# Optimization experiments

Measured on AMD Instinct MI355X. Metric: run time of the kernel, lower is better.

The kernel has to match this reference:

```python
import jax, jax.numpy as jnp
import numpy as np

N, E, H = 50000, 800000, 128
HQ = H // 4  # 32


def _mlp(x, w1, b1, w2, b2):
    return jax.nn.relu(x @ w1 + b1) @ w2 + b2


def setup_inputs() -> dict:
    key = jax.random.key(0)
    ks = jax.random.split(key, 16)

    def lin(k, fan_in, fan_out):
        lim = 1.0 / np.sqrt(fan_in)
        kw, kb = jax.random.split(k)
        w = jax.random.uniform(kw, (fan_in, fan_out), jnp.float32, -lim, lim)
        b = jax.random.uniform(kb, (fan_out,), jnp.float32, -lim, lim)
        return w, b

    x = jax.random.normal(ks[0], (N, H), jnp.float32)
    pos = jax.random.normal(ks[1], (N, 3), jnp.float32)
    edge_index = jax.random.randint(ks[2], (2, E), 0, N, jnp.int64)

    pw1, pb1 = lin(ks[3], 3, HQ)
    pw2, pb2 = lin(ks[4], HQ, HQ)
    mw1, mb1 = lin(ks[5], 2 * H + HQ, H)
    mw2, mb2 = lin(ks[6], H, H)
    uw1, ub1 = lin(ks[7], 2 * H, H)
    uw2, ub2 = lin(ks[8], H, H)

    return dict(x=x, pos=pos, edge_index=edge_index,
                pw1=pw1, pb1=pb1, pw2=pw2, pb2=pb2,
                mw1=mw1, mb1=mb1, mw2=mw2, mb2=mb2,
                uw1=uw1, ub1=ub1, uw2=uw2, ub2=ub2)


def reference(x, pos, edge_index,
              pw1, pb1, pw2, pb2,
              mw1, mb1, mw2, mb2,
              uw1, ub1, uw2, ub2):
    row, col = edge_index[0], edge_index[1]
    # position features from relative positions [E, 3] -> [E, H//4]
    pos_feat = _mlp(pos[row] - pos[col], pw1, pb1, pw2, pb2)
    # per-edge messages [E, 2H + H//4] -> [E, H]
    msg_in = jnp.concatenate([x[row], x[col], pos_feat], axis=-1)
    messages = _mlp(msg_in, mw1, mb1, mw2, mb2)
    # scatter-add messages into destination nodes (index_add on col)
    agg = jax.ops.segment_sum(messages, col, num_segments=x.shape[0])
    # node update [N, 2H] -> [N, H]
    return _mlp(jnp.concatenate([x, agg], axis=-1), uw1, ub1, uw2, ub2)
```

## Files before the change

kernel.cpp:

```cpp
#include <hip/hip_runtime.h>
#include <hip/hip_bf16.h>

#define NN 50000
#define NE 800000
#define HD 128
#define SCAN_CHUNK 1024
#define SCAN_BLOCKS ((NN + SCAN_CHUNK - 1) / SCAN_CHUNK)
#define NB_NODE 1024
#define EPB ((NE + NB_NODE - 1) / NB_NODE)
#define NB_SSUB 256
#define NB_SCAT (NB_SSUB * 8)
#define EPC ((NE + NB_SSUB - 1) / NB_SSUB)
#define NPG (NN / 8)

typedef __attribute__((ext_vector_type(8))) short s16x8;
typedef __attribute__((ext_vector_type(4))) float f32x4;

static __device__ __forceinline__ unsigned short f2bf(float f) {
    unsigned int u = __float_as_uint(f);
    u = (u + 0x7FFFu + ((u >> 16) & 1u)) >> 16;
    return (unsigned short)u;
}
static __device__ __forceinline__ float bf2f(unsigned short h) {
    return __uint_as_float(((unsigned int)h) << 16);
}
static __device__ __forceinline__ unsigned int f2bf2(float lo, float hi) {
    __hip_bfloat162 h = __float22bfloat162_rn(make_float2(lo, hi));
    return *reinterpret_cast<unsigned int*>(&h);
}

#define WFENCE() do { asm volatile("s_waitcnt lgkmcnt(0)" ::: "memory"); \
                      __builtin_amdgcn_sched_barrier(0); } while (0)

__global__ __launch_bounds__(256, 3) void node_kernel(
    const float* __restrict__ x, const float* __restrict__ mw1,
    const float* __restrict__ mb1, const float* __restrict__ pb2,
    const int* __restrict__ ei,
    unsigned short* __restrict__ xa, unsigned short* __restrict__ xb,
    float* __restrict__ aggH, int* __restrict__ cnt)
{
    __shared__ __align__(16) unsigned short sB[128 * 136];
    __shared__ __align__(16) unsigned short sSt[4][16 * 132];
    __shared__ int sIdx64;

    int bid = blockIdx.x;
    int tid = threadIdx.x;

    {
        f32x4 z = {0.f, 0.f, 0.f, 0.f};
        const int total4 = NN * HD / 4;
        for (int i = bid * 256 + tid; i < total4; i += NB_NODE * 256)
            ((f32x4*)aggH)[i] = z;
    }
    if (tid == 0) {
        int z = 1;
        for (int k = 0; k < 16; ++k) if (ei[2 * k + 1] != 0) z = 0;
        sIdx64 = z;
    }
    int half = bid & 1;
    for (int idx = tid; idx < 128 * 128; idx += 256) {
        int c = idx & 127, k = idx >> 7;
        sB[c * 136 + k] = f2bf(mw1[(half * 128 + k) * 128 + c]);
    }
    __syncthreads();

    {
        int he0 = bid * EPB;
        int he1 = he0 + EPB; if (he1 > NE) he1 = NE;
        if (sIdx64) {
            for (int e = he0 + tid; e < he1; e += 256)
                atomicAdd(&cnt[ei[2 * NE + 2 * e]], 1);
        } else {
            for (int e = he0 + tid; e < he1; e += 256)
                atomicAdd(&cnt[ei[NE + e]], 1);
        }
    }

    int lane = tid & 63, wv = tid >> 6;
    int r16 = lane & 15, g4 = lane >> 4;
    unsigned short* st = sSt[wv];
    unsigned short* dst = half ? xb : xa;

    float bcr[8];
    #pragma unroll
    for (int tc = 0; tc < 8; ++tc) bcr[tc] = 0.f;
    if (half) {
        #pragma unroll
        for (int tc = 0; tc < 8; ++tc) bcr[tc] = mb1[tc * 16 + r16];
        for (int i = 0; i < 32; ++i) {
            float pv = pb2[i];
            #pragma unroll
            for (int tc = 0; tc < 8; ++tc)
                bcr[tc] = fmaf(pv, mw1[(256 + i) * 128 + tc * 16 + r16], bcr[tc]);
        }
    }

    const int NT = NN / 16;
    const int nb = NB_NODE >> 1;
    const int nbid = bid >> 1;

    for (int t = nbid * 4 + wv; t < NT; t += nb * 4) {
        int r0 = t * 16;
        int row = r0 + r16;
        s16x8 a[4];
        #pragma unroll
        for (int ks = 0; ks < 4; ++ks) {
            const float* p = &x[(size_t)row * HD + ks * 32 + g4 * 8];
            float4 v0 = *(const float4*)p;
            float4 v1 = *(const float4*)(p + 4);
            union { s16x8 v; unsigned int u[4]; } av;
            av.u[0] = f2bf2(v0.x, v0.y); av.u[1] = f2bf2(v0.z, v0.w);
            av.u[2] = f2bf2(v1.x, v1.y); av.u[3] = f2bf2(v1.z, v1.w);
            a[ks] = av.v;
        }
        float hold[4];
        #pragma unroll
        for (int tc = 0; tc < 8; ++tc) {
            int col = tc * 16 + r16;
            float bv = bcr[tc];
            f32x4 acc = {bv, bv, bv, bv};
            #pragma unroll
            for (int ks = 0; ks < 4; ++ks) {
                s16x8 b = *(const s16x8*)&sB[col * 136 + ks * 32 + g4 * 8];
                acc = __builtin_amdgcn_mfma_f32_16x16x32_bf16(a[ks], b, acc, 0, 0, 0);
            }
            if ((tc & 1) == 0) {
                #pragma unroll
                for (int j = 0; j < 4; ++j) hold[j] = acc[j];
            } else {
                #pragma unroll
                for (int j = 0; j < 4; ++j)
                    *(unsigned int*)&st[(g4 * 4 + j) * 132 + r16 * 8 + (tc - 1)] =
                        f2bf2(hold[j], acc[j]);
            }
        }
        WFENCE();
        #pragma unroll
        for (int i = 0; i < 4; ++i) {
            int idx = i * 512 + lane * 8;
            int rr = idx >> 7, cc = idx & 127;
            *(s16x8*)&dst[(size_t)(r0 + rr) * HD + cc] = *(const s16x8*)&st[rr * 132 + cc];
        }
        WFENCE();
    }
}

__global__ void scan1_kernel(const int* __restrict__ cnt, int* __restrict__ cursor,
                             int* __restrict__ bsum)
{
    __shared__ int tot[256];
    int b = blockIdx.x, t = threadIdx.x;
    int i0 = b * SCAN_CHUNK + t * 4;
    int v[4];
    #pragma unroll
    for (int k = 0; k < 4; ++k) v[k] = (i0 + k < NN) ? cnt[i0 + k] : 0;
    tot[t] = v[0] + v[1] + v[2] + v[3];
    __syncthreads();
    if (t == 0) {
        int run = 0;
        for (int i = 0; i < 256; ++i) { int x = tot[i]; tot[i] = run; run += x; }
        bsum[b] = run;
    }
    __syncthreads();
    int p = tot[t];
    #pragma unroll
    for (int k = 0; k < 4; ++k) {
        if (i0 + k < NN) cursor[i0 + k] = p;
        p += v[k];
    }
}

__global__ void scan3_kernel(int* __restrict__ cursor, const int* __restrict__ bsum,
                             const int* __restrict__ cnt, int* __restrict__ sC)
{
    __shared__ int sCarry;
    int b = blockIdx.x, t = threadIdx.x;
    if (t == 0) {
        int run = 0;
        for (int i = 0; i < b; ++i) run += bsum[i];
        sCarry = run;
    }
    __syncthreads();
    int carry = sCarry;
    int i0 = b * SCAN_CHUNK + t * 4;
    #pragma unroll
    for (int k = 0; k < 4; ++k) {
        int i = i0 + k;
        if (i < NN) {
            int s = cursor[i] + carry;
            cursor[i] = s;
            int n = cnt[i];
            for (int j = 0; j < n; ++j) sC[s + j] = i;
        }
    }
}

__global__ void scatterprep_kernel(
    const int* __restrict__ ei, int* __restrict__ cursor, int* __restrict__ sR,
    const float* __restrict__ pw2, const float* __restrict__ mw1,
    const float* __restrict__ mw2, const float* __restrict__ mb2,
    const float* __restrict__ uw1,
    float* __restrict__ Wpc, float* __restrict__ W3, float* __restrict__ b3)
{
    __shared__ int sIdx64;
    int bid = blockIdx.x, tid = threadIdx.x;

    if (bid >= NB_SCAT) {
        int rb = bid - NB_SCAT;
        if (rb == 64) {
            for (int idx = tid; idx < 32 * 128; idx += 256) {
                int j = idx >> 7, k = idx & 127;
                float s = 0.f;
                #pragma unroll 8
                for (int i = 0; i < 32; ++i) s += pw2[j * 32 + i] * mw1[(256 + i) * 128 + k];
                Wpc[idx] = s;
            }
            return;
        }
        int idx = rb * 256 + tid;
        {
            int k = idx >> 7, j = idx & 127;
            float s = 0.f;
            #pragma unroll 4
            for (int c = 0; c < 128; ++c)
                s += mw2[k * 128 + c] * uw1[(128 + c) * 128 + j];
            W3[idx] = s;
        }
        if (rb == 0 && tid < 128) {
            int j = tid;
            float s = 0.f;
            #pragma unroll 4
            for (int c = 0; c < 128; ++c)
                s += mb2[c] * uw1[(128 + c) * 128 + j];
            b3[j] = s;
        }
        return;
    }

    if (tid == 0) {
        int z = 1;
        for (int k = 0; k < 16; ++k) if (ei[2 * k + 1] != 0) z = 0;
        sIdx64 = z;
    }
    __syncthreads();

    int g = bid & 7;
    int sub = bid >> 3;
    int clo = g * NPG;
    int chi = (g == 7) ? NN : clo + NPG;
    int e0 = sub * EPC;
    int e1 = e0 + EPC; if (e1 > NE) e1 = NE;

    if (sIdx64) {
        for (int e = e0 + tid; e < e1; e += 256) {
            int c = ei[2 * NE + 2 * e];
            if (c >= clo && c < chi) {
                int r = ei[2 * e];
                int p = atomicAdd(&cursor[c], 1);
                sR[p] = r;
            }
        }
    } else {
        for (int e = e0 + tid; e < e1; e += 256) {
            int c = ei[NE + e];
            if (c >= clo && c < chi) {
                int r = ei[e];
                int p = atomicAdd(&cursor[c], 1);
                sR[p] = r;
            }
        }
    }
}

__global__ __launch_bounds__(256, 3) void edge_kernel(
    const float* __restrict__ pos,
    const int* __restrict__ sR, const int* __restrict__ sC,
    const float* __restrict__ pw1, const float* __restrict__ pb1,
    const unsigned short* __restrict__ xa, const unsigned short* __restrict__ xb,
    const float* __restrict__ Wpc,
    float* __restrict__ aggH)
{
    __shared__ __align__(16) unsigned short sT[4][16 * 136];

    int tid = threadIdx.x;
    int lane = tid & 63, wv = tid >> 6;
    int r16 = lane & 15, g4 = lane >> 4;
    unsigned short* stg = sT[wv];

    s16x8 wr[8];
    #pragma unroll
    for (int tc = 0; tc < 8; ++tc) {
        s16x8 w;
        #pragma unroll
        for (int i = 0; i < 8; ++i)
            w[i] = (short)f2bf(Wpc[(g4 * 8 + i) * 128 + tc * 16 + r16]);
        wr[tc] = w;
    }
    float pw10[8], pw11[8], pw12[8], pb1r[8];
    #pragma unroll
    for (int i = 0; i < 8; ++i) {
        int k = g4 * 8 + i;
        pw10[i] = pw1[k]; pw11[i] = pw1[32 + k]; pw12[i] = pw1[64 + k];
        pb1r[i] = pb1[k];
    }

    const int NW = gridDim.x * 4;
    const int NT = NE / 16;
    int gw = blockIdx.x * 4 + wv;
    if (gw >= NT) return;

    int2 rc, rcN;
    rc.x = sR[gw * 16 + r16];
    rc.y = sC[gw * 16 + r16];
    rcN = rc;
    if (gw + NW < NT) {
        rcN.x = sR[(gw + NW) * 16 + r16];
        rcN.y = sC[(gw + NW) * 16 + r16];
    }
    float dp0 = pos[rc.x * 3 + 0] - pos[rc.y * 3 + 0];
    float dp1 = pos[rc.x * 3 + 1] - pos[rc.y * 3 + 1];
    float dp2 = pos[rc.x * 3 + 2] - pos[rc.y * 3 + 2];
    s16x8 ga[4], gb[4];
    #pragma unroll
    for (int j = 0; j < 4; ++j) {
        int gx = __shfl(rc.x, g4 * 4 + j, 64);
        int gy = __shfl(rc.y, g4 * 4 + j, 64);
        ga[j] = *(const s16x8*)&xa[(size_t)gx * HD + r16 * 8];
        gb[j] = *(const s16x8*)&xb[(size_t)gy * HD + r16 * 8];
    }

    for (int t = gw; t < NT; t += NW) {
        bool hn  = (t + NW) < NT;
        bool hn2 = (t + 2 * NW) < NT;

        union { s16x8 v; unsigned int u[4]; } apf;
        #pragma unroll
        for (int i2 = 0; i2 < 4; ++i2) {
            int i = 2 * i2;
            float v0 = fmaf(dp0, pw10[i], fmaf(dp1, pw11[i], fmaf(dp2, pw12[i], pb1r[i])));
            float v1 = fmaf(dp0, pw10[i+1], fmaf(dp1, pw11[i+1], fmaf(dp2, pw12[i+1], pb1r[i+1])));
            apf.u[i2] = f2bf2(fmaxf(v0, 0.f), fmaxf(v1, 0.f));
        }

        float hold[4];
        #pragma unroll
        for (int tc = 0; tc < 8; ++tc) {
            f32x4 acc;
            #pragma unroll
            for (int j = 0; j < 4; ++j)
                acc[j] = bf2f((unsigned short)ga[j][tc]) + bf2f((unsigned short)gb[j][tc]);
            acc = __builtin_amdgcn_mfma_f32_16x16x32_bf16(apf.v, wr[tc], acc, 0, 0, 0);
            if ((tc & 1) == 0) {
                #pragma unroll
                for (int j = 0; j < 4; ++j) hold[j] = fmaxf(acc[j], 0.f);
            } else {
                #pragma unroll
                for (int j = 0; j < 4; ++j)
                    *(unsigned int*)&stg[(g4 * 4 + j) * 136 + r16 * 8 + (tc - 1)] =
                        f2bf2(hold[j], fmaxf(acc[j], 0.f));
            }
        }
        WFENCE();

        if (hn) {
            #pragma unroll
            for (int j = 0; j < 4; ++j) {
                int gx = __shfl(rcN.x, g4 * 4 + j, 64);
                int gy = __shfl(rcN.y, g4 * 4 + j, 64);
                ga[j] = *(const s16x8*)&xa[(size_t)gx * HD + r16 * 8];
                gb[j] = *(const s16x8*)&xb[(size_t)gy * HD + r16 * 8];
            }
        }

        int2 rcN2 = rcN;
        if (hn2) {
            int i2x = (t + 2 * NW) * 16 + r16;
            rcN2.x = sR[i2x];
            rcN2.y = sC[i2x];
        }
        float dp0N = 0.f, dp1N = 0.f, dp2N = 0.f;
        if (hn) {
            dp0N = pos[rcN.x * 3 + 0] - pos[rcN.y * 3 + 0];
            dp1N = pos[rcN.x * 3 + 1] - pos[rcN.y * 3 + 1];
            dp2N = pos[rcN.x * 3 + 2] - pos[rcN.y * 3 + 2];
        }

        {
            int tb = __builtin_amdgcn_readfirstlane(t);
            const int* __restrict__ scp = sC + tb * 16;
            int p0 = (lane & 15) * 8 + (lane >> 4);
            int p1 = p0 + 4;
            int cur = scp[0];
            float run0 = bf2f(stg[p0]);
            float run1 = bf2f(stg[p1]);
            #pragma unroll
            for (int e = 1; e < 16; ++e) {
                int c = scp[e];
                float v0 = bf2f(stg[e * 136 + p0]);
                float v1 = bf2f(stg[e * 136 + p1]);
                if (c != cur) {
                    unsafeAtomicAdd(&aggH[(size_t)cur * HD + lane], run0);
                    unsafeAtomicAdd(&aggH[(size_t)cur * HD + lane + 64], run1);
                    cur = c; run0 = v0; run1 = v1;
                } else { run0 += v0; run1 += v1; }
            }
            unsafeAtomicAdd(&aggH[(size_t)cur * HD + lane], run0);
            unsafeAtomicAdd(&aggH[(size_t)cur * HD + lane + 64], run1);
        }
        WFENCE();

        rc = rcN; rcN = rcN2; dp0 = dp0N; dp1 = dp1N; dp2 = dp2N;
    }
}

__global__ __launch_bounds__(768, 1) void upd_kernel(
    const float* __restrict__ x, const float* __restrict__ aggH,
    const int* __restrict__ cnt,
    const float* __restrict__ uw1, const float* __restrict__ ub1,
    const float* __restrict__ W3, const float* __restrict__ b3,
    const float* __restrict__ uw2, const float* __restrict__ ub2,
    float* __restrict__ out)
{
    __shared__ __align__(16) unsigned short sB1a[128 * 136];
    __shared__ __align__(16) unsigned short sW3l[128 * 136];
    __shared__ __align__(16) unsigned short sB2[128 * 136];
    __shared__ __align__(16) unsigned short sSt[12][16 * 136];

    int tid = threadIdx.x;
    for (int idx = tid; idx < 128 * 128; idx += 768) {
        int c = idx & 127, k = idx >> 7;
        sB1a[c * 136 + k] = f2bf(uw1[k * 128 + c]);
        sW3l[c * 136 + k] = f2bf(W3[k * 128 + c]);
        sB2[c * 136 + k]  = f2bf(uw2[k * 128 + c]);
    }
    __syncthreads();

    int lane = tid & 63, wv = tid >> 6;
    int r16 = lane & 15, g4 = lane >> 4;
    unsigned short* st = sSt[wv];
    float ub1r[8], ub2r[8], b3r[8];
    #pragma unroll
    for (int tc = 0; tc < 8; ++tc) {
        ub1r[tc] = ub1[tc * 16 + r16];
        ub2r[tc] = ub2[tc * 16 + r16];
        b3r[tc]  = b3[tc * 16 + r16];
    }

    const int NT = NN / 16;
    for (int t = blockIdx.x * 12 + wv; t < NT; t += gridDim.x * 12) {
        int r0 = t * 16;
        int row = r0 + r16;
        s16x8 a[8];
        #pragma unroll
        for (int ks = 0; ks < 8; ++ks) {
            const float* p = (ks < 4) ? &x[(size_t)row * HD + ks * 32 + g4 * 8]
                                      : &aggH[(size_t)row * HD + (ks - 4) * 32 + g4 * 8];
            float4 v0 = *(const float4*)p;
            float4 v1 = *(const float4*)(p + 4);
            union { s16x8 v; unsigned int u[4]; } av;
            av.u[0] = f2bf2(v0.x, v0.y); av.u[1] = f2bf2(v0.z, v0.w);
            av.u[2] = f2bf2(v1.x, v1.y); av.u[3] = f2bf2(v1.z, v1.w);
            a[ks] = av.v;
        }
        float cn[4];
        #pragma unroll
        for (int j = 0; j < 4; ++j) cn[j] = (float)cnt[r0 + g4 * 4 + j];

        #pragma unroll
        for (int tc = 0; tc < 8; ++tc) {
            int col = tc * 16 + r16;
            f32x4 acc;
            #pragma unroll
            for (int j = 0; j < 4; ++j) acc[j] = ub1r[tc] + cn[j] * b3r[tc];
            #pragma unroll
            for (int ks = 0; ks < 4; ++ks) {
                s16x8 b = *(const s16x8*)&sB1a[col * 136 + ks * 32 + g4 * 8];
                acc = __builtin_amdgcn_mfma_f32_16x16x32_bf16(a[ks], b, acc, 0, 0, 0);
            }
            #pragma unroll
            for (int ks = 4; ks < 8; ++ks) {
                s16x8 b = *(const s16x8*)&sW3l[col * 136 + (ks - 4) * 32 + g4 * 8];
                acc = __builtin_amdgcn_mfma_f32_16x16x32_bf16(a[ks], b, acc, 0, 0, 0);
            }
            #pragma unroll
            for (int j = 0; j < 4; ++j)
                st[(g4 * 4 + j) * 136 + col] = f2bf(fmaxf(acc[j], 0.f));
        }
        WFENCE();
        s16x8 a2[4];
        #pragma unroll
        for (int ks = 0; ks < 4; ++ks)
            a2[ks] = *(const s16x8*)&st[r16 * 136 + ks * 32 + g4 * 8];
        WFENCE();
        #pragma unroll
        for (int tc = 0; tc < 8; ++tc) {
            int col = tc * 16 + r16;
            float bv = ub2r[tc];
            f32x4 acc = {bv, bv, bv, bv};
            #pragma unroll
            for (int ks = 0; ks < 4; ++ks) {
                s16x8 b = *(const s16x8*)&sB2[col * 136 + ks * 32 + g4 * 8];
                acc = __builtin_amdgcn_mfma_f32_16x16x32_bf16(a2[ks], b, acc, 0, 0, 0);
            }
            #pragma unroll
            for (int j = 0; j < 4; ++j)
                out[(size_t)(r0 + g4 * 4 + j) * HD + col] = acc[j];
        }
    }
}

extern "C" void kernel_launch(void* const* d_in, const int* in_sizes, int n_in,
                              void* d_out, int out_size, void* d_ws, size_t ws_size,
                              hipStream_t stream)
{
    const float* x   = (const float*)d_in[0];
    const float* pos = (const float*)d_in[1];
    const int*   ei  = (const int*)d_in[2];
    const float* pw1 = (const float*)d_in[3];
    const float* pb1 = (const float*)d_in[4];
    const float* pw2 = (const float*)d_in[5];
    const float* pb2 = (const float*)d_in[6];
    const float* mw1 = (const float*)d_in[7];
    const float* mb1 = (const float*)d_in[8];
    const float* mw2 = (const float*)d_in[9];
    const float* mb2 = (const float*)d_in[10];
    const float* uw1 = (const float*)d_in[11];
    const float* ub1 = (const float*)d_in[12];
    const float* uw2 = (const float*)d_in[13];
    const float* ub2 = (const float*)d_in[14];
    float* out = (float*)d_out;

    char* ws = (char*)d_ws;
    float*          aggH   = (float*)(ws);
    unsigned short* xa     = (unsigned short*)(ws + 25600000);
    unsigned short* xb     = (unsigned short*)(ws + 38400000);
    float*          Wpc    = (float*)(ws + 51200000);
    int*            cnt    = (int*)(ws + 51216896);
    int*            cursor = (int*)(ws + 51417600);
    int*            bsum   = (int*)(ws + 51618304);
    int*            sR     = (int*)(ws + 51618560);
    int*            sC     = (int*)(ws + 54818560);
    float*          W3     = (float*)(ws + 58018560);
    float*          b3     = (float*)(ws + 58084096);

    hipMemsetAsync(cnt, 0, NN * sizeof(int), stream);
    node_kernel<<<NB_NODE, 256, 0, stream>>>(x, mw1, mb1, pb2, ei, xa, xb, aggH, cnt);
    scan1_kernel<<<SCAN_BLOCKS, 256, 0, stream>>>(cnt, cursor, bsum);
    scan3_kernel<<<SCAN_BLOCKS, 256, 0, stream>>>(cursor, bsum, cnt, sC);
    scatterprep_kernel<<<NB_SCAT + 65, 256, 0, stream>>>(
        ei, cursor, sR, pw2, mw1, mw2, mb2, uw1, Wpc, W3, b3);
    edge_kernel<<<768, 256, 0, stream>>>(pos, sR, sC, pw1, pb1, xa, xb, Wpc, aggH);
    upd_kernel<<<256, 768, 0, stream>>>(x, aggH, cnt, uw1, ub1, W3, b3, uw2, ub2, out);
}
```

Baseline: 212.2 us.

## Double-buffer edge-tile gathers two tiles ahead in message kernel

```diff
diff --git a/kernel.cpp b/kernel.cpp
--- a/kernel.cpp
+++ b/kernel.cpp
@@ -309,108 +309,116 @@
     int gw = blockIdx.x * 4 + wv;
     if (gw >= NT) return;
 
-    int2 rc, rcN;
-    rc.x = sR[gw * 16 + r16];
-    rc.y = sC[gw * 16 + r16];
-    rcN = rc;
-    if (gw + NW < NT) {
-        rcN.x = sR[(gw + NW) * 16 + r16];
-        rcN.y = sC[(gw + NW) * 16 + r16];
-    }
-    float dp0 = pos[rc.x * 3 + 0] - pos[rc.y * 3 + 0];
-    float dp1 = pos[rc.x * 3 + 1] - pos[rc.y * 3 + 1];
-    float dp2 = pos[rc.x * 3 + 2] - pos[rc.y * 3 + 2];
-    s16x8 ga[4], gb[4];
-    #pragma unroll
-    for (int j = 0; j < 4; ++j) {
-        int gx = __shfl(rc.x, g4 * 4 + j, 64);
-        int gy = __shfl(rc.y, g4 * 4 + j, 64);
-        ga[j] = *(const s16x8*)&xa[(size_t)gx * HD + r16 * 8];
-        gb[j] = *(const s16x8*)&xb[(size_t)gy * HD + r16 * 8];
-    }
-
-    for (int t = gw; t < NT; t += NW) {
-        bool hn  = (t + NW) < NT;
-        bool hn2 = (t + 2 * NW) < NT;
-
-        union { s16x8 v; unsigned int u[4]; } apf;
-        #pragma unroll
-        for (int i2 = 0; i2 < 4; ++i2) {
-            int i = 2 * i2;
-            float v0 = fmaf(dp0, pw10[i], fmaf(dp1, pw11[i], fmaf(dp2, pw12[i], pb1r[i])));
-            float v1 = fmaf(dp0, pw10[i+1], fmaf(dp1, pw11[i+1], fmaf(dp2, pw12[i+1], pb1r[i+1])));
-            apf.u[i2] = f2bf2(fmaxf(v0, 0.f), fmaxf(v1, 0.f));
-        }
-
-        float hold[4];
-        #pragma unroll
-        for (int tc = 0; tc < 8; ++tc) {
-            f32x4 acc;
-            #pragma unroll
-            for (int j = 0; j < 4; ++j)
-                acc[j] = bf2f((unsigned short)ga[j][tc]) + bf2f((unsigned short)gb[j][tc]);
-            acc = __builtin_amdgcn_mfma_f32_16x16x32_bf16(apf.v, wr[tc], acc, 0, 0, 0);
-            if ((tc & 1) == 0) {
-                #pragma unroll
-                for (int j = 0; j < 4; ++j) hold[j] = fmaxf(acc[j], 0.f);
-            } else {
-                #pragma unroll
-                for (int j = 0; j < 4; ++j)
-                    *(unsigned int*)&stg[(g4 * 4 + j) * 136 + r16 * 8 + (tc - 1)] =
-                        f2bf2(hold[j], fmaxf(acc[j], 0.f));
-            }
-        }
-        WFENCE();
-
-        if (hn) {
-            #pragma unroll
-            for (int j = 0; j < 4; ++j) {
-                int gx = __shfl(rcN.x, g4 * 4 + j, 64);
-                int gy = __shfl(rcN.y, g4 * 4 + j, 64);
-                ga[j] = *(const s16x8*)&xa[(size_t)gx * HD + r16 * 8];
-                gb[j] = *(const s16x8*)&xb[(size_t)gy * HD + r16 * 8];
-            }
-        }
-
-        int2 rcN2 = rcN;
-        if (hn2) {
-            int i2x = (t + 2 * NW) * 16 + r16;
-            rcN2.x = sR[i2x];
-            rcN2.y = sC[i2x];
-        }
-        float dp0N = 0.f, dp1N = 0.f, dp2N = 0.f;
-        if (hn) {
-            dp0N = pos[rcN.x * 3 + 0] - pos[rcN.y * 3 + 0];
-            dp1N = pos[rcN.x * 3 + 1] - pos[rcN.y * 3 + 1];
-            dp2N = pos[rcN.x * 3 + 2] - pos[rcN.y * 3 + 2];
-        }
-
-        {
-            int tb = __builtin_amdgcn_readfirstlane(t);
-            const int* __restrict__ scp = sC + tb * 16;
-            int p0 = (lane & 15) * 8 + (lane >> 4);
-            int p1 = p0 + 4;
-            int cur = scp[0];
-            float run0 = bf2f(stg[p0]);
-            float run1 = bf2f(stg[p1]);
-            #pragma unroll
-            for (int e = 1; e < 16; ++e) {
-                int c = scp[e];
-                float v0 = bf2f(stg[e * 136 + p0]);
-                float v1 = bf2f(stg[e * 136 + p1]);
-                if (c != cur) {
-                    unsafeAtomicAdd(&aggH[(size_t)cur * HD + lane], run0);
-                    unsafeAtomicAdd(&aggH[(size_t)cur * HD + lane + 64], run1);
-                    cur = c; run0 = v0; run1 = v1;
-                } else { run0 += v0; run1 += v1; }
-            }
-            unsafeAtomicAdd(&aggH[(size_t)cur * HD + lane], run0);
-            unsafeAtomicAdd(&aggH[(size_t)cur * HD + lane + 64], run1);
-        }
-        WFENCE();
-
-        rc = rcN; rcN = rcN2; dp0 = dp0N; dp1 = dp1N; dp2 = dp2N;
-    }
+#define LOAD_META(M, TT)                                                    \
+    { int tt_ = (TT) < NT ? (TT) : NT - 1;                                  \
+      M.x = sR[tt_ * 16 + r16]; M.y = sC[tt_ * 16 + r16]; }
+
+#define POSDIFF(D0, D1, D2, M)                                              \
+    D0 = pos[M.x * 3 + 0] - pos[M.y * 3 + 0];                               \
+    D1 = pos[M.x * 3 + 1] - pos[M.y * 3 + 1];                               \
+    D2 = pos[M.x * 3 + 2] - pos[M.y * 3 + 2];
+
+#define GATHER_TILE(GA, GB, M)                                              \
+    _Pragma("unroll")                                                       \
+    for (int j = 0; j < 4; ++j) {                                           \
+        int gx = __shfl(M.x, g4 * 4 + j, 64);                               \
+        int gy = __shfl(M.y, g4 * 4 + j, 64);                               \
+        GA[j] = *(const s16x8*)&xa[(size_t)gx * HD + r16 * 8];              \
+        GB[j] = *(const s16x8*)&xb[(size_t)gy * HD + r16 * 8];              \
+    }
+
+#define GEMM1_TILE(GA, GB, D0, D1, D2)                                      \
+    {                                                                       \
+        union { s16x8 v; unsigned int u[4]; } apf;                          \
+        _Pragma("unroll")                                                   \
+        for (int i2 = 0; i2 < 4; ++i2) {                                    \
+            int i = 2 * i2;                                                 \
+            float v0_ = fmaf(D0, pw10[i], fmaf(D1, pw11[i], fmaf(D2, pw12[i], pb1r[i])));          \
+            float v1_ = fmaf(D0, pw10[i+1], fmaf(D1, pw11[i+1], fmaf(D2, pw12[i+1], pb1r[i+1])));  \
+            apf.u[i2] = f2bf2(fmaxf(v0_, 0.f), fmaxf(v1_, 0.f));            \
+        }                                                                   \
+        float hold[4];                                                      \
+        _Pragma("unroll")                                                   \
+        for (int tc = 0; tc < 8; ++tc) {                                    \
+            f32x4 acc;                                                      \
+            _Pragma("unroll")                                               \
+            for (int j = 0; j < 4; ++j)                                     \
+                acc[j] = bf2f((unsigned short)GA[j][tc]) + bf2f((unsigned short)GB[j][tc]);        \
+            acc = __builtin_amdgcn_mfma_f32_16x16x32_bf16(apf.v, wr[tc], acc, 0, 0, 0);            \
+            if ((tc & 1) == 0) {                                            \
+                _Pragma("unroll")                                           \
+                for (int j = 0; j < 4; ++j) hold[j] = fmaxf(acc[j], 0.f);   \
+            } else {                                                        \
+                _Pragma("unroll")                                           \
+                for (int j = 0; j < 4; ++j)                                 \
+                    *(unsigned int*)&stg[(g4 * 4 + j) * 136 + r16 * 8 + (tc - 1)] =                \
+                        f2bf2(hold[j], fmaxf(acc[j], 0.f));                 \
+            }                                                               \
+        }                                                                   \
+    }
+
+#define SEGRED_TILE(TT)                                                     \
+    {                                                                       \
+        int tb_ = __builtin_amdgcn_readfirstlane(TT);                       \
+        const int* __restrict__ scp = sC + tb_ * 16;                        \
+        int p0 = (lane & 15) * 8 + (lane >> 4);                             \
+        int p1 = p0 + 4;                                                    \
+        int cur = scp[0];                                                   \
+        float run0 = bf2f(stg[p0]);                                         \
+        float run1 = bf2f(stg[p1]);                                         \
+        _Pragma("unroll")                                                   \
+        for (int e = 1; e < 16; ++e) {                                      \
+            int c = scp[e];                                                 \
+            float v0_ = bf2f(stg[e * 136 + p0]);                            \
+            float v1_ = bf2f(stg[e * 136 + p1]);                            \
+            if (c != cur) {                                                 \
+                unsafeAtomicAdd(&aggH[(size_t)cur * HD + lane], run0);      \
+                unsafeAtomicAdd(&aggH[(size_t)cur * HD + lane + 64], run1); \
+                cur = c; run0 = v0_; run1 = v1_;                            \
+            } else { run0 += v0_; run1 += v1_; }                            \
+        }                                                                   \
+        unsafeAtomicAdd(&aggH[(size_t)cur * HD + lane], run0);              \
+        unsafeAtomicAdd(&aggH[(size_t)cur * HD + lane + 64], run1);         \
+    }
+
+    int2 m0, m1, m2, m3;
+    LOAD_META(m0, gw);
+    LOAD_META(m1, gw + NW);
+    LOAD_META(m2, gw + 2 * NW);
+    LOAD_META(m3, gw + 3 * NW);
+    s16x8 ga0[4], gb0[4], ga1[4], gb1[4];
+    GATHER_TILE(ga0, gb0, m0);
+    GATHER_TILE(ga1, gb1, m1);
+    float dpA0, dpA1, dpA2, dpB0, dpB1, dpB2;
+    POSDIFF(dpA0, dpA1, dpA2, m0);
+    POSDIFF(dpB0, dpB1, dpB2, m1);
+
+    for (int t = gw; t < NT; t += 2 * NW) {
+        GEMM1_TILE(ga0, gb0, dpA0, dpA1, dpA2);
+        WFENCE();
+        GATHER_TILE(ga0, gb0, m2);
+        int2 m4; LOAD_META(m4, t + 4 * NW);
+        POSDIFF(dpA0, dpA1, dpA2, m2);
+        SEGRED_TILE(t);
+        WFENCE();
+
+        GEMM1_TILE(ga1, gb1, dpB0, dpB1, dpB2);
+        WFENCE();
+        GATHER_TILE(ga1, gb1, m3);
+        int2 m5; LOAD_META(m5, t + 5 * NW);
+        POSDIFF(dpB0, dpB1, dpB2, m3);
+        if (t + NW < NT) {
+            SEGRED_TILE(t + NW);
+            WFENCE();
+        }
+        m2 = m4; m3 = m5;
+    }
+
+#undef LOAD_META
+#undef POSDIFF
+#undef GATHER_TILE
+#undef GEMM1_TILE
+#undef SEGRED_TILE
 }
 
 __global__ __launch_bounds__(768, 1) void upd_kernel(
```

Result: no change. 214.1 us (+0.9%).
